# Kernel optimization log

Measured on AMD Instinct MI355X. Metric: run time of the kernel, lower is better.

Reference implementation:

```python
import jax, jax.numpy as jnp
import numpy as np

N = 20000   # nodes
E = 40000   # directed edges
F_IN = 13   # dataset.num_features
G = 1000    # graphs in batch
DIMS = [(13, 32), (32, 64), (64, 64)]  # (M_in, M_out) per NNConv layer


def setup_inputs() -> dict:
    key = jax.random.key(0)
    ks = list(jax.random.split(key, 32))
    inp = {}
    inp["x"] = jax.random.normal(ks[0], (N, F_IN), jnp.float32)
    inp["edge_index"] = jax.random.randint(ks[1], (2, E), 0, N, dtype=jnp.int32)
    inp["edge_attr"] = jax.random.uniform(ks[2], (E, 5), dtype=jnp.float32)
    inp["batch"] = jnp.sort(jax.random.randint(ks[3], (N,), 0, G, dtype=jnp.int32))
    i = 4
    for l, (mi, mo) in enumerate(DIMS):
        inp[f"w1_{l}"] = jax.random.normal(ks[i], (5, 128), jnp.float32) / np.sqrt(5.0).astype(np.float32); i += 1
        inp[f"b1_{l}"] = jnp.zeros((128,), jnp.float32)
        inp[f"w2_{l}"] = jax.random.normal(ks[i], (128, mi * mo), jnp.float32) / np.sqrt(128.0).astype(np.float32); i += 1
        inp[f"b2_{l}"] = jnp.zeros((mi * mo,), jnp.float32)
        inp[f"root_{l}"] = jax.random.normal(ks[i], (mi, mo), jnp.float32) / np.sqrt(float(mi)).astype(np.float32); i += 1
        inp[f"bias_{l}"] = jnp.zeros((mo,), jnp.float32)
    inp["fc1_w"] = jax.random.normal(ks[i], (64, 32), jnp.float32) / 8.0; i += 1
    inp["fc1_b"] = jnp.zeros((32,), jnp.float32)
    inp["fc2_w"] = jax.random.normal(ks[i], (32, 16), jnp.float32) / np.sqrt(32.0).astype(np.float32); i += 1
    inp["fc2_b"] = jnp.zeros((16,), jnp.float32)
    inp["fc3_w"] = jax.random.normal(ks[i], (16, 1), jnp.float32) / 4.0; i += 1
    inp["fc3_b"] = jnp.zeros((1,), jnp.float32)
    return inp


def _nnconv(x, src, dst, edge_attr, w1, b1, w2, b2, root, bias, mi, mo):
    # edge MLP: [E,5] -> [E,128] -> [E, mi*mo] per-edge weight matrices
    h = jax.nn.relu(edge_attr @ w1 + b1)
    We = (h @ w2 + b2).reshape(-1, mi, mo)          # [E, mi, mo]
    msg = jnp.einsum('ei,eio->eo', x[src], We)      # gather + per-edge matmul
    agg = jax.ops.segment_sum(msg, dst, num_segments=x.shape[0])  # scatter-add
    return x @ root + agg + bias                    # NNConv root weight + bias


def _forward(x, edge_index, edge_attr, batch, convs, fc1_w, fc1_b, fc2_w, fc2_b, fc3_w, fc3_b):
    src, dst = edge_index[0], edge_index[1]
    for (mi, mo), (w1, b1, w2, b2, root, bias) in zip(DIMS, convs):
        x = jax.nn.elu(_nnconv(x, src, dst, edge_attr, w1, b1, w2, b2, root, bias, mi, mo))
    # scatter_mean pooling over graphs
    sums = jax.ops.segment_sum(x, batch, num_segments=G)
    cnt = jax.ops.segment_sum(jnp.ones((x.shape[0],), x.dtype), batch, num_segments=G)
    xg = sums / jnp.maximum(cnt, 1.0)[:, None]
    xg = jax.nn.elu(xg @ fc1_w + fc1_b)
    xg = jax.nn.elu(xg @ fc2_w + fc2_b)
    return (xg @ fc3_w + fc3_b).reshape(-1)


def reference(x, edge_index, edge_attr, batch,
              w1_0, b1_0, w2_0, b2_0, root_0, bias_0,
              w1_1, b1_1, w2_1, b2_1, root_1, bias_1,
              w1_2, b1_2, w2_2, b2_2, root_2, bias_2,
              fc1_w, fc1_b, fc2_w, fc2_b, fc3_w, fc3_b):
    convs = [(w1_0, b1_0, w2_0, b2_0, root_0, bias_0),
             (w1_1, b1_1, w2_1, b2_1, root_1, bias_1),
             (w1_2, b1_2, w2_2, b2_2, root_2, bias_2)]
    return _forward(x, edge_index, edge_attr, batch, convs,
                    fc1_w, fc1_b, fc2_w, fc2_b, fc3_w, fc3_b)
```

## Files before the change

### kernel.cpp

```cpp
#include <hip/hip_runtime.h>
#include <stdint.h>
#include <math.h>

typedef _Float16 half8_t __attribute__((ext_vector_type(8)));
typedef float floatx4 __attribute__((ext_vector_type(4)));

#define NN 20000
#define NE 40000
#define NG 1000
#define NBLK 157
#define NSPLIT 4

__global__ __launch_bounds__(256) void prep_fused_kernel(
    const float* __restrict__ x, _Float16* __restrict__ e16,
    const float* __restrict__ w2a, const float* __restrict__ b2a, _Float16* __restrict__ oa,
    const float* __restrict__ w2b, const float* __restrict__ b2b, _Float16* __restrict__ ob,
    const float* __restrict__ w2c, const float* __restrict__ b2c, _Float16* __restrict__ oc,
    int* __restrict__ deg)
{
  if (blockIdx.x < 1250) {
    int idx = blockIdx.x * 256 + threadIdx.x;
    int n = idx >> 4, i = idx & 15;
    e16[idx] = (i < 13) ? (_Float16)x[(size_t)n * 13 + i] : (_Float16)0.f;
    return;
  }
  if (blockIdx.x >= 1680) {
    int n = (blockIdx.x - 1680) * 256 + threadIdx.x;
    if (n < NN) deg[n] = 0;
    return;
  }
  const int TOT0 = 68 * 2 * 64, TOT1 = 132 * 4 * 64, TOT2 = 264 * 4 * 64;
  int idx = (blockIdx.x - 1250) * 256 + threadIdx.x;
  const float *w2, *b2; _Float16* op; int mi, mo, mpsh, CT;
  if (idx < TOT0) { w2 = w2a; b2 = b2a; op = oa; mi = 13; mo = 32; mpsh = 4; CT = 2; }
  else if (idx < TOT0 + TOT1) { idx -= TOT0; w2 = w2b; b2 = b2b; op = ob; mi = 32; mo = 64; mpsh = 5; CT = 4; }
  else if (idx < TOT0 + TOT1 + TOT2) { idx -= TOT0 + TOT1; w2 = w2c; b2 = b2c; op = oc; mi = 64; mo = 64; mpsh = 6; CT = 4; }
  else return;
  int l = idx & 63;
  int ct = (idx >> 6) % CT;
  int c = idx / (64 * CT);
  int q = l >> 4;
  int n = ct * 16 + (l & 15);
  int mask = (1 << mpsh) - 1;
  half8_t v;
#pragma unroll
  for (int j = 0; j < 8; ++j) {
    int r = c * 32 + q * 8 + j;
    int k = r >> mpsh, i = r & mask;
    float f = 0.f;
    if (i < mi) {
      if (k < 128) f = w2[(size_t)(k * mi + i) * mo + n];
      else if (k == 128) f = b2[(size_t)i * mo + n];
    }
    v[j] = (_Float16)f;
  }
  *(half8_t*)(op + (size_t)idx * 8) = v;
}

__global__ __launch_bounds__(256) void deg_kernel(const int* __restrict__ dst, int* __restrict__ deg) {
  int e = blockIdx.x * 256 + threadIdx.x;
  if (e < NE) atomicAdd(&deg[dst[e]], 1);
}

__global__ __launch_bounds__(1024) void scan_kernel(
    const int* __restrict__ deg, int* __restrict__ row_ptr, int* __restrict__ cursor)
{
  constexpr int CH = 20;
  __shared__ int wsum[16];
  int t = threadIdx.x;
  int lane = t & 63, w = t >> 6;
  int base = t * CH;
  int local[CH];
#pragma unroll
  for (int i = 0; i < CH; ++i) {
    int n = base + i;
    local[i] = (n < NN) ? deg[n] : 0;
  }
  int s = 0;
#pragma unroll
  for (int i = 0; i < CH; ++i) s += local[i];
  int sc = s;
#pragma unroll
  for (int d = 1; d < 64; d <<= 1) {
    int v = __shfl_up(sc, d, 64);
    if (lane >= d) sc += v;
  }
  if (lane == 63) wsum[w] = sc;
  __syncthreads();
  if (w == 0 && lane < 16) {
    int v = wsum[lane];
    int scc = v;
#pragma unroll
    for (int d = 1; d < 16; d <<= 1) {
      int u = __shfl_up(scc, d, 64);
      if (lane >= d) scc += u;
    }
    wsum[lane] = scc - v;
  }
  __syncthreads();
  int run = wsum[w] + (sc - s);
#pragma unroll
  for (int i = 0; i < CH; ++i) {
    int n = base + i;
    if (n < NN) { row_ptr[n] = run; cursor[n] = run; run += local[i]; }
    else if (n == NN) row_ptr[NN] = run;
  }
}

__global__ __launch_bounds__(256) void fill_kernel(
    const int* __restrict__ dst, int* __restrict__ cursor, int* __restrict__ eids)
{
  int e = blockIdx.x * 256 + threadIdx.x;
  if (e < NE) { int p = atomicAdd(&cursor[dst[e]], 1); eids[p] = e; }
}

template <int MIP, int MO, int NCC, int KCNT>
__global__ __launch_bounds__(256, 3) void msg9_kernel(
    const float* __restrict__ ea, const float* __restrict__ w1,
    const float* __restrict__ b1, const _Float16* __restrict__ xe,
    const int* __restrict__ src,
    const _Float16* __restrict__ w2h, _Float16* __restrict__ msgp)
{
  constexpr int EPB = 256;
  constexpr int CT = MO / 16;
  constexpr int CHB = CT * 1024;
  constexpr int XLSS = MIP + 8;
  constexpr int HSTW = KCNT | 1;
  constexpr int XV = (MIP == 64) ? 2 : 1;
  constexpr int NU4 = MIP / 8;
  constexpr int XB = EPB * XLSS * 2;
  constexpr int HB = EPB * HSTW * 4;
  constexpr int SBYTES = (XB > HB) ? XB : HB;

  __shared__ char sb[SBYTES];
  __shared__ uint4 wsb[2][CHB / 16];
  __shared__ float w1s[5 * 128 + 128];

  _Float16* sxb = (_Float16*)sb;
  unsigned* hls = (unsigned*)sb;

  const int t = threadIdx.x;
  const int wave = t >> 6, lane = t & 63;
  const int l15 = lane & 15, q = lane >> 4;
  const int split = blockIdx.x / NBLK;
  const int e0 = (blockIdx.x % NBLK) * EPB;
  const int c0 = NCC * split;
  const int kg0 = KCNT * split;

  {
    int eg = e0 + t; if (eg >= NE) eg = NE - 1;
    const uint4* xr = (const uint4*)(xe + (size_t)src[eg] * MIP);
    uint4* xd = (uint4*)(sxb + t * XLSS);
#pragma unroll
    for (int u = 0; u < NU4; ++u) xd[u] = xr[u];
  }
  float ear[5];
  {
    int eg = e0 + t; if (eg >= NE) eg = NE - 1;
#pragma unroll
    for (int j = 0; j < 5; ++j) ear[j] = ea[(size_t)eg * 5 + j];
  }
  for (int i = t; i < 768; i += 256) w1s[i] = (i < 640) ? w1[i] : b1[i - 640];
  __syncthreads();

  const int wbase = wave * 64;
  half8_t xf[4][XV];
#pragma unroll
  for (int s = 0; s < 4; ++s) {
    int el = wbase + s * 16 + l15;
    int i0 = (MIP == 16) ? (q & 1) * 8 : q * 8;
    xf[s][0] = *(const half8_t*)(sxb + el * XLSS + i0);
    if constexpr (MIP == 64)
      xf[s][XV - 1] = *(const half8_t*)(sxb + el * XLSS + 32 + q * 8);
  }
  __syncthreads();

  for (int kl = 0; kl < KCNT; ++kl) {
    int kg = kg0 + kl;
    float v;
    if (kg < 128) {
      v = w1s[640 + kg];
#pragma unroll
      for (int j = 0; j < 5; ++j) v = fmaf(ear[j], w1s[j * 128 + kg], v);
      v = fmaxf(v, 0.f);
    } else v = (kg == 128) ? 1.f : 0.f;
    union { _Float16 f; unsigned short u; } cv; cv.f = (_Float16)v;
    hls[t * HSTW + kl] = (unsigned)cv.u * 0x10001u;
  }
  __syncthreads();

  floatx4 acc[4][CT];
#pragma unroll
  for (int s = 0; s < 4; ++s)
#pragma unroll
    for (int b = 0; b < CT; ++b) acc[s][b] = (floatx4){0.f, 0.f, 0.f, 0.f};

  const char* wgp = (const char*)w2h + (size_t)c0 * CHB;
  uint4 r4; uint2 r2;
  if constexpr (CT == 4) r4 = *(const uint4*)(wgp + t * 16);
  else r2 = *(const uint2*)(wgp + t * 8);

#pragma unroll 2
  for (int cc = 0; cc < NCC; ++cc) {
    if constexpr (CT == 4) wsb[cc & 1][t] = r4;
    else ((uint2*)wsb[cc & 1])[t] = r2;
    __syncthreads();
    if (cc + 1 < NCC) {
      if constexpr (CT == 4) r4 = *(const uint4*)(wgp + (size_t)(cc + 1) * CHB + t * 16);
      else r2 = *(const uint2*)(wgp + (size_t)(cc + 1) * CHB + t * 8);
    }
    const _Float16* wb = (const _Float16*)wsb[cc & 1];
    half8_t bf[CT];
#pragma unroll
    for (int b = 0; b < CT; ++b)
      bf[b] = *(const half8_t*)(wb + (b * 64 + lane) * 8);
    int kl;
    if constexpr (MIP == 64) kl = cc >> 1;
    else if constexpr (MIP == 32) kl = cc;
    else kl = 2 * cc + (q >> 1);
#pragma unroll
    for (int s = 0; s < 4; ++s) {
      _Float16 hv = *(const _Float16*)(hls + (wbase + s * 16 + l15) * HSTW + kl);
      half8_t af;
      if constexpr (MIP == 64) af = xf[s][cc & 1] * hv;
      else af = xf[s][0] * hv;
#pragma unroll
      for (int b = 0; b < CT; ++b)
        acc[s][b] = __builtin_amdgcn_mfma_f32_16x16x32_f16(af, bf[b], acc[s][b], 0, 0, 0);
    }
  }

  _Float16* mp = msgp + (size_t)split * NE * MO;
#pragma unroll
  for (int s = 0; s < 4; ++s) {
    int rowb = wbase + s * 16 + q * 4;
#pragma unroll
    for (int b = 0; b < CT; ++b) {
      int n = b * 16 + l15;
#pragma unroll
      for (int r = 0; r < 4; ++r) {
        int row = rowb + r;
        int e = e0 + row;
        if (e < NE) mp[(size_t)e * MO + n] = (_Float16)acc[s][b][r];
      }
    }
  }
}

template <int MIN_, int XST, int MO, int FINAL>
__global__ __launch_bounds__(256) void gather_kernel(
    const _Float16* __restrict__ e16in, const float* __restrict__ root,
    const float* __restrict__ bias, const int* __restrict__ row_ptr,
    const int* __restrict__ eids, const _Float16* __restrict__ msgp,
    _Float16* __restrict__ oute, float* __restrict__ outf)
{
  constexpr int NPB = 256 / MO;
  int n = blockIdx.x * NPB + threadIdx.x / MO;
  int o = threadIdx.x % MO;
  if (n >= NN) return;
  float a = bias[o];
#pragma unroll
  for (int i = 0; i < MIN_; ++i)
    a = fmaf((float)e16in[(size_t)n * XST + i], root[i * MO + o], a);
  int r0 = row_ptr[n], r1 = row_ptr[n + 1];
  for (int j = r0; j < r1; ++j) {
    int e = eids[j];
#pragma unroll
    for (int s = 0; s < NSPLIT; ++s)
      a += (float)msgp[((size_t)s * NE + e) * MO + o];
  }
  if constexpr (FINAL) {
    outf[(size_t)n * MO + o] = a;
  } else {
    float v = a > 0.f ? a : (expf(a) - 1.f);
    oute[(size_t)n * MO + o] = (_Float16)v;
  }
}

__global__ __launch_bounds__(64) void pool_fc_kernel(
    const float* __restrict__ xn2, const int* __restrict__ batch,
    const float* __restrict__ f1w, const float* __restrict__ f1b,
    const float* __restrict__ f2w, const float* __restrict__ f2b,
    const float* __restrict__ f3w, const float* __restrict__ f3b,
    float* __restrict__ out)
{
  __shared__ float xg[64]; __shared__ float a1[32]; __shared__ float a2[16];
  int g = blockIdx.x, t = threadIdx.x;
  int lo = 0, hi = NN;
  while (lo < hi) { int m = (lo + hi) >> 1; if (batch[m] < g) lo = m + 1; else hi = m; }
  int start = lo; hi = NN;
  while (lo < hi) { int m = (lo + hi) >> 1; if (batch[m] <= g) lo = m + 1; else hi = m; }
  int end = lo;
  float acc = 0.f;
  for (int n = start; n < end; ++n) {
    float v = xn2[(size_t)n * 64 + t];
    acc += v > 0.f ? v : (expf(v) - 1.f);
  }
  float c = (end > start) ? (float)(end - start) : 1.f;
  xg[t] = acc / c;
  __syncthreads();
  if (t < 32) {
    float a = f1b[t];
    for (int i = 0; i < 64; ++i) a = fmaf(xg[i], f1w[i * 32 + t], a);
    a1[t] = a > 0.f ? a : (expf(a) - 1.f);
  }
  __syncthreads();
  if (t < 16) {
    float a = f2b[t];
    for (int i = 0; i < 32; ++i) a = fmaf(a1[i], f2w[i * 16 + t], a);
    a2[t] = a > 0.f ? a : (expf(a) - 1.f);
  }
  __syncthreads();
  if (t == 0) {
    float a = f3b[0];
    for (int i = 0; i < 16; ++i) a = fmaf(a2[i], f3w[i], a);
    out[g] = a;
  }
}

extern "C" void kernel_launch(void* const* d_in, const int* in_sizes, int n_in,
                              void* d_out, int out_size, void* d_ws, size_t ws_size,
                              hipStream_t stream)
{
  const float* x_in  = (const float*)d_in[0];
  const int*   ei    = (const int*)d_in[1];
  const float* ea    = (const float*)d_in[2];
  const int*   batch = (const int*)d_in[3];
  const float* W1[3] = {(const float*)d_in[4],  (const float*)d_in[10], (const float*)d_in[16]};
  const float* B1[3] = {(const float*)d_in[5],  (const float*)d_in[11], (const float*)d_in[17]};
  const float* W2[3] = {(const float*)d_in[6],  (const float*)d_in[12], (const float*)d_in[18]};
  const float* B2[3] = {(const float*)d_in[7],  (const float*)d_in[13], (const float*)d_in[19]};
  const float* RT[3] = {(const float*)d_in[8],  (const float*)d_in[14], (const float*)d_in[20]};
  const float* BS[3] = {(const float*)d_in[9],  (const float*)d_in[15], (const float*)d_in[21]};
  const float* f1w = (const float*)d_in[22]; const float* f1b = (const float*)d_in[23];
  const float* f2w = (const float*)d_in[24]; const float* f2b = (const float*)d_in[25];
  const float* f3w = (const float*)d_in[26]; const float* f3b = (const float*)d_in[27];

  char* ws = (char*)d_ws;
  size_t off = 0;
  auto alloc = [&](size_t bytes) { void* p = ws + off; off += (bytes + 255) & ~(size_t)255; return p; };
  float*    xn2   = (float*)alloc((size_t)NN * 64 * 4);
  _Float16* e16_0 = (_Float16*)alloc((size_t)NN * 16 * 2);
  _Float16* e16_1 = (_Float16*)alloc((size_t)NN * 32 * 2);
  _Float16* e16_2 = (_Float16*)alloc((size_t)NN * 64 * 2);
  _Float16* w2h0  = (_Float16*)alloc((size_t)68 * 2048);
  _Float16* w2h1  = (_Float16*)alloc((size_t)132 * 4096);
  _Float16* w2h2  = (_Float16*)alloc((size_t)264 * 4096);
  _Float16* msgp  = (_Float16*)alloc((size_t)NSPLIT * NE * 64 * 2);
  int*      deg     = (int*)alloc((size_t)NN * 4);
  int*      row_ptr = (int*)alloc((size_t)(NN + 1) * 4);
  int*      cursor  = (int*)alloc((size_t)NN * 4);
  int*      eids    = (int*)alloc((size_t)NE * 4);

  const int* srcp = ei;
  const int* dstp = ei + NE;

  prep_fused_kernel<<<1680 + (NN + 255) / 256, 256, 0, stream>>>(
      x_in, e16_0, W2[0], B2[0], w2h0, W2[1], B2[1], w2h1, W2[2], B2[2], w2h2, deg);
  deg_kernel<<<(NE + 255) / 256, 256, 0, stream>>>(dstp, deg);
  scan_kernel<<<1, 1024, 0, stream>>>(deg, row_ptr, cursor);
  fill_kernel<<<(NE + 255) / 256, 256, 0, stream>>>(dstp, cursor, eids);

  msg9_kernel<16, 32, 17, 34><<<NBLK * NSPLIT, 256, 0, stream>>>(
      ea, W1[0], B1[0], e16_0, srcp, w2h0, msgp);
  gather_kernel<13, 16, 32, 0><<<(NN + 7) / 8, 256, 0, stream>>>(
      e16_0, RT[0], BS[0], row_ptr, eids, msgp, e16_1, xn2);

  msg9_kernel<32, 64, 33, 33><<<NBLK * NSPLIT, 256, 0, stream>>>(
      ea, W1[1], B1[1], e16_1, srcp, w2h1, msgp);
  gather_kernel<32, 32, 64, 0><<<(NN + 3) / 4, 256, 0, stream>>>(
      e16_1, RT[1], BS[1], row_ptr, eids, msgp, e16_2, xn2);

  msg9_kernel<64, 64, 66, 33><<<NBLK * NSPLIT, 256, 0, stream>>>(
      ea, W1[2], B1[2], e16_2, srcp, w2h2, msgp);
  gather_kernel<64, 64, 64, 1><<<(NN + 3) / 4, 256, 0, stream>>>(
      e16_2, RT[2], BS[2], row_ptr, eids, msgp, e16_2, xn2);

  pool_fc_kernel<<<NG, 64, 0, stream>>>(xn2, batch, f1w, f1b, f2w, f2b, f3w, f3b, (float*)d_out);
}
```

Measured before the change: 302.6 us.

## Double the K-split, load gathered x directly to registers, prefetch two weight chunks ahead

Raises the hidden-dimension split from 4 to 8, so each message block handles half as many K chunks and twice as many blocks launch. The padded weight buffers and prep grid grow to match. The gathered source-node features now load straight from global memory into MFMA fragment registers instead of being staged through shared memory, which drops one barrier. The weight-chunk prefetch is now two stages deep. The h values are stored as packed halves in a transposed layout. In exchange, twice as many partial message buffers must be written and summed by the gather kernels, and the global gathers are less coalesced.

```diff
diff --git a/kernel.cpp b/kernel.cpp
--- a/kernel.cpp
+++ b/kernel.cpp
@@ -9,7 +9,7 @@
 #define NE 40000
 #define NG 1000
 #define NBLK 157
-#define NSPLIT 4
+#define NSPLIT 8
 
 __global__ __launch_bounds__(256) void prep_fused_kernel(
     const float* __restrict__ x, _Float16* __restrict__ e16,
@@ -24,12 +24,12 @@
     e16[idx] = (i < 13) ? (_Float16)x[(size_t)n * 13 + i] : (_Float16)0.f;
     return;
   }
-  if (blockIdx.x >= 1680) {
-    int n = (blockIdx.x - 1680) * 256 + threadIdx.x;
+  if (blockIdx.x >= 1694) {
+    int n = (blockIdx.x - 1694) * 256 + threadIdx.x;
     if (n < NN) deg[n] = 0;
     return;
   }
-  const int TOT0 = 68 * 2 * 64, TOT1 = 132 * 4 * 64, TOT2 = 264 * 4 * 64;
+  const int TOT0 = 72 * 2 * 64, TOT1 = 136 * 4 * 64, TOT2 = 272 * 4 * 64;
   int idx = (blockIdx.x - 1250) * 256 + threadIdx.x;
   const float *w2, *b2; _Float16* op; int mi, mo, mpsh, CT;
   if (idx < TOT0) { w2 = w2a; b2 = b2a; op = oa; mi = 13; mo = 32; mpsh = 4; CT = 2; }
@@ -124,20 +124,11 @@
   constexpr int EPB = 256;
   constexpr int CT = MO / 16;
   constexpr int CHB = CT * 1024;
-  constexpr int XLSS = MIP + 8;
-  constexpr int HSTW = KCNT | 1;
   constexpr int XV = (MIP == 64) ? 2 : 1;
-  constexpr int NU4 = MIP / 8;
-  constexpr int XB = EPB * XLSS * 2;
-  constexpr int HB = EPB * HSTW * 4;
-  constexpr int SBYTES = (XB > HB) ? XB : HB;
-
-  __shared__ char sb[SBYTES];
+
   __shared__ uint4 wsb[2][CHB / 16];
+  __shared__ _Float16 h16[KCNT * EPB];
   __shared__ float w1s[5 * 128 + 128];
-
-  _Float16* sxb = (_Float16*)sb;
-  unsigned* hls = (unsigned*)sb;
 
   const int t = threadIdx.x;
   const int wave = t >> 6, lane = t & 63;
@@ -147,13 +138,28 @@
   const int c0 = NCC * split;
   const int kg0 = KCNT * split;
 
-  {
-    int eg = e0 + t; if (eg >= NE) eg = NE - 1;
-    const uint4* xr = (const uint4*)(xe + (size_t)src[eg] * MIP);
-    uint4* xd = (uint4*)(sxb + t * XLSS);
-#pragma unroll
-    for (int u = 0; u < NU4; ++u) xd[u] = xr[u];
-  }
+  const char* wgp = (const char*)w2h + (size_t)c0 * CHB;
+  uint4 ra4, rb4; uint2 ra2, rb2;
+  if constexpr (CT == 4) {
+    ra4 = *(const uint4*)(wgp + t * 16);
+    rb4 = *(const uint4*)(wgp + CHB + t * 16);
+  } else {
+    ra2 = *(const uint2*)(wgp + t * 8);
+    rb2 = *(const uint2*)(wgp + CHB + t * 8);
+  }
+
+  const int wbase = wave * 64;
+  half8_t xf[4][XV];
+#pragma unroll
+  for (int s = 0; s < 4; ++s) {
+    int eg = e0 + wbase + s * 16 + l15; if (eg >= NE) eg = NE - 1;
+    const _Float16* xr = xe + (size_t)src[eg] * MIP;
+    int i0 = (MIP == 16) ? (q & 1) * 8 : q * 8;
+    xf[s][0] = *(const half8_t*)(xr + i0);
+    if constexpr (MIP == 64)
+      xf[s][XV - 1] = *(const half8_t*)(xr + 32 + q * 8);
+  }
+
   float ear[5];
   {
     int eg = e0 + t; if (eg >= NE) eg = NE - 1;
@@ -161,18 +167,6 @@
     for (int j = 0; j < 5; ++j) ear[j] = ea[(size_t)eg * 5 + j];
   }
   for (int i = t; i < 768; i += 256) w1s[i] = (i < 640) ? w1[i] : b1[i - 640];
-  __syncthreads();
-
-  const int wbase = wave * 64;
-  half8_t xf[4][XV];
-#pragma unroll
-  for (int s = 0; s < 4; ++s) {
-    int el = wbase + s * 16 + l15;
-    int i0 = (MIP == 16) ? (q & 1) * 8 : q * 8;
-    xf[s][0] = *(const half8_t*)(sxb + el * XLSS + i0);
-    if constexpr (MIP == 64)
-      xf[s][XV - 1] = *(const half8_t*)(sxb + el * XLSS + 32 + q * 8);
-  }
   __syncthreads();
 
   for (int kl = 0; kl < KCNT; ++kl) {
@@ -184,8 +178,7 @@
       for (int j = 0; j < 5; ++j) v = fmaf(ear[j], w1s[j * 128 + kg], v);
       v = fmaxf(v, 0.f);
     } else v = (kg == 128) ? 1.f : 0.f;
-    union { _Float16 f; unsigned short u; } cv; cv.f = (_Float16)v;
-    hls[t * HSTW + kl] = (unsigned)cv.u * 0x10001u;
+    h16[kl * EPB + t] = (_Float16)v;
   }
   __syncthreads();
 
@@ -194,21 +187,21 @@
   for (int s = 0; s < 4; ++s)
 #pragma unroll
     for (int b = 0; b < CT; ++b) acc[s][b] = (floatx4){0.f, 0.f, 0.f, 0.f};
-
-  const char* wgp = (const char*)w2h + (size_t)c0 * CHB;
-  uint4 r4; uint2 r2;
-  if constexpr (CT == 4) r4 = *(const uint4*)(wgp + t * 16);
-  else r2 = *(const uint2*)(wgp + t * 8);
 
 #pragma unroll 2
   for (int cc = 0; cc < NCC; ++cc) {
-    if constexpr (CT == 4) wsb[cc & 1][t] = r4;
-    else ((uint2*)wsb[cc & 1])[t] = r2;
+    const bool odd = (cc & 1) != 0;
+    if constexpr (CT == 4) wsb[cc & 1][t] = odd ? rb4 : ra4;
+    else ((uint2*)wsb[cc & 1])[t] = odd ? rb2 : ra2;
+    if (cc + 2 < NCC) {
+      const char* np = wgp + (size_t)(cc + 2) * CHB;
+      if constexpr (CT == 4) {
+        if (odd) rb4 = *(const uint4*)(np + t * 16); else ra4 = *(const uint4*)(np + t * 16);
+      } else {
+        if (odd) rb2 = *(const uint2*)(np + t * 8); else ra2 = *(const uint2*)(np + t * 8);
+      }
+    }
     __syncthreads();
-    if (cc + 1 < NCC) {
-      if constexpr (CT == 4) r4 = *(const uint4*)(wgp + (size_t)(cc + 1) * CHB + t * 16);
-      else r2 = *(const uint2*)(wgp + (size_t)(cc + 1) * CHB + t * 8);
-    }
     const _Float16* wb = (const _Float16*)wsb[cc & 1];
     half8_t bf[CT];
 #pragma unroll
@@ -220,7 +213,7 @@
     else kl = 2 * cc + (q >> 1);
 #pragma unroll
     for (int s = 0; s < 4; ++s) {
-      _Float16 hv = *(const _Float16*)(hls + (wbase + s * 16 + l15) * HSTW + kl);
+      _Float16 hv = h16[kl * EPB + wbase + s * 16 + l15];
       half8_t af;
       if constexpr (MIP == 64) af = xf[s][cc & 1] * hv;
       else af = xf[s][0] * hv;
@@ -343,9 +336,9 @@
   _Float16* e16_0 = (_Float16*)alloc((size_t)NN * 16 * 2);
   _Float16* e16_1 = (_Float16*)alloc((size_t)NN * 32 * 2);
   _Float16* e16_2 = (_Float16*)alloc((size_t)NN * 64 * 2);
-  _Float16* w2h0  = (_Float16*)alloc((size_t)68 * 2048);
-  _Float16* w2h1  = (_Float16*)alloc((size_t)132 * 4096);
-  _Float16* w2h2  = (_Float16*)alloc((size_t)264 * 4096);
+  _Float16* w2h0  = (_Float16*)alloc((size_t)72 * 2048);
+  _Float16* w2h1  = (_Float16*)alloc((size_t)136 * 4096);
+  _Float16* w2h2  = (_Float16*)alloc((size_t)272 * 4096);
   _Float16* msgp  = (_Float16*)alloc((size_t)NSPLIT * NE * 64 * 2);
   int*      deg     = (int*)alloc((size_t)NN * 4);
   int*      row_ptr = (int*)alloc((size_t)(NN + 1) * 4);
@@ -355,23 +348,23 @@
   const int* srcp = ei;
   const int* dstp = ei + NE;
 
-  prep_fused_kernel<<<1680 + (NN + 255) / 256, 256, 0, stream>>>(
+  prep_fused_kernel<<<1694 + (NN + 255) / 256, 256, 0, stream>>>(
       x_in, e16_0, W2[0], B2[0], w2h0, W2[1], B2[1], w2h1, W2[2], B2[2], w2h2, deg);
   deg_kernel<<<(NE + 255) / 256, 256, 0, stream>>>(dstp, deg);
   scan_kernel<<<1, 1024, 0, stream>>>(deg, row_ptr, cursor);
   fill_kernel<<<(NE + 255) / 256, 256, 0, stream>>>(dstp, cursor, eids);
 
-  msg9_kernel<16, 32, 17, 34><<<NBLK * NSPLIT, 256, 0, stream>>>(
+  msg9_kernel<16, 32, 9, 18><<<NBLK * NSPLIT, 256, 0, stream>>>(
       ea, W1[0], B1[0], e16_0, srcp, w2h0, msgp);
   gather_kernel<13, 16, 32, 0><<<(NN + 7) / 8, 256, 0, stream>>>(
       e16_0, RT[0], BS[0], row_ptr, eids, msgp, e16_1, xn2);
 
-  msg9_kernel<32, 64, 33, 33><<<NBLK * NSPLIT, 256, 0, stream>>>(
+  msg9_kernel<32, 64, 17, 17><<<NBLK * NSPLIT, 256, 0, stream>>>(
       ea, W1[1], B1[1], e16_1, srcp, w2h1, msgp);
   gather_kernel<32, 32, 64, 0><<<(NN + 3) / 4, 256, 0, stream>>>(
       e16_1, RT[1], BS[1], row_ptr, eids, msgp, e16_2, xn2);
 
-  msg9_kernel<64, 64, 66, 33><<<NBLK * NSPLIT, 256, 0, stream>>>(
+  msg9_kernel<64, 64, 34, 17><<<NBLK * NSPLIT, 256, 0, stream>>>(
       ea, W1[2], B1[2], e16_2, srcp, w2h2, msgp);
   gather_kernel<64, 64, 64, 1><<<(NN + 3) / 4, 256, 0, stream>>>(
       e16_2, RT[2], BS[2], row_ptr, eids, msgp, e16_2, xn2);
```

Measured after the change: 304.8 us. Within noise of the previous version (+0.7%).
